# Performance work log

Measured on AMD Instinct MI355X. Metric: run time of the kernel, lower is better.

## Reference

```python
import jax, jax.numpy as jnp
import numpy as np

M, C = 100000, 24
LINE_W, LENGTH_W, REPROJ_W = 0.0, 0.0, 1.0  # forward() default weights


def setup_inputs() -> dict:
    ks = jax.random.split(jax.random.key(0), 8)
    # 3 pole markers per frame, centered ~5m in front of cameras (positive depth)
    pole3d = 0.5 * jax.random.normal(ks[0], (M, 3, 3), jnp.float32) + jnp.array([0.0, 0.0, 5.0], jnp.float32)
    # intrinsics: fx=fy~1000, principal point ~(960,540)
    fx = 1000.0 + 10.0 * jax.random.normal(ks[1], (C,), jnp.float32)
    fy = 1000.0 + 10.0 * jax.random.normal(ks[2], (C,), jnp.float32)
    u0 = 960.0 + 5.0 * jax.random.normal(ks[3], (C,), jnp.float32)
    v0 = 540.0 + 5.0 * jax.random.normal(ks[4], (C,), jnp.float32)
    K = jnp.zeros((C, 3, 3), jnp.float32)
    K = K.at[:, 0, 0].set(fx).at[:, 1, 1].set(fy).at[:, 0, 2].set(u0).at[:, 1, 2].set(v0).at[:, 2, 2].set(1.0)
    dist = 0.01 * jax.random.normal(ks[5], (C, 5), jnp.float32)  # k1,k2,p1,p2,k3
    R = jnp.eye(3, dtype=jnp.float32)[None] + 0.01 * jax.random.normal(ks[6], (C, 3, 3), jnp.float32)
    t = 0.1 * jax.random.normal(ks[7], (C, 3), jnp.float32)
    # detected pixels in a 1920x1080 frame
    pole2d = jax.random.uniform(jax.random.fold_in(ks[0], 1), (M, C, 3, 2), jnp.float32) * jnp.array([1920.0, 1080.0], jnp.float32)
    # visibility mask; guarantee >=1 visible camera per frame (matches non-empty loss_reproj)
    mask = jax.random.randint(jax.random.fold_in(ks[0], 2), (M, C), 0, 2, jnp.int32).at[:, 0].set(1)
    pole = jnp.array([0.5, 0.5], jnp.float32)  # [d1, d2] in meters
    return {"pole3d": pole3d, "pole2d": pole2d, "K": K, "dist": dist, "R": R, "t": t, "pole": pole, "mask": mask}


def _project(X, K, R, t, dist):
    # X: [M,P,3] world points; outputs pixels [M,C,P,2]
    xc = jnp.einsum('cij,mpj->mcpi', R, X) + t[None, :, None, :]   # camera frame
    xn = xc[..., :2] / xc[..., 2:3]                                # perspective divide
    x0, x1 = xn[..., 0], xn[..., 1]
    r2 = x0 * x0 + x1 * x1
    k1, k2, p1, p2, k3 = (dist[:, i][None, :, None] for i in range(5))
    radial = 1.0 + k1 * r2 + k2 * r2 * r2 + k3 * r2 * r2 * r2
    xu = x0 * radial + 2.0 * p1 * x0 * x1 + p2 * (r2 + 2.0 * x0 * x0)
    yu = x1 * radial + p1 * (r2 + 2.0 * x1 * x1) + 2.0 * p2 * x0 * x1
    fx = K[:, 0, 0][None, :, None]; fy = K[:, 1, 1][None, :, None]
    u0 = K[:, 0, 2][None, :, None]; v0 = K[:, 1, 2][None, :, None]
    return jnp.stack([fx * xu + u0, fy * yu + v0], axis=-1)


def reference(pole3d, pole2d, K, dist, R, t, pole, mask):
    d1, d2 = pole[0], pole[1]
    dsum = d1 + d2
    # wand geometry loss per frame
    expect_mid = (d2 * pole3d[:, 0] + d1 * pole3d[:, 2]) / dsum            # [M,3]
    loss_line = jnp.linalg.norm(pole3d[:, 1] - expect_mid, axis=-1)        # [M]
    loss_length = jnp.abs(jnp.linalg.norm(pole3d[:, 0] - pole3d[:, 2], axis=-1) - dsum)
    loss_wand = LINE_W * loss_line + LENGTH_W * loss_length                # [M]
    # reprojection loss
    proj = _project(pole3d, K, R, t, dist)                                 # [M,C,3,2]
    per_cam = REPROJ_W * jnp.linalg.norm(pole2d - proj, axis=-1).mean(axis=-1)  # [M,C]
    m = mask.astype(per_cam.dtype)
    loss_reproj = (per_cam * m).sum(axis=-1) / m.sum(axis=-1)              # masked mean over cams
    return jnp.mean(loss_wand + loss_reproj)
```

## Files before the change

kernel.cpp:

```cpp
#include <hip/hip_runtime.h>

#define MM 100000
#define CC 24
#define BLK 256
#define WPB (BLK / 64)
#define GRID 1280
#define NW (GRID * WPB)
#define NP (MM / 2)

struct Pack {
    float2 a0, a1, a2;
    float  w;
    float  q[9];
};

__device__ __forceinline__ Pack load_pack(
    const float* __restrict__ pole3d, const float* __restrict__ pole2d,
    const int* __restrict__ mask, int m, int c, float active)
{
    Pack pk;
    const float2* pd = (const float2*)(pole2d + ((size_t)m * CC + c) * 6);
    pk.a0 = pd[0]; pk.a1 = pd[1]; pk.a2 = pd[2];
    pk.w  = active * (float)mask[(size_t)m * CC + c];
    const float* q = pole3d + (size_t)m * 9;
    #pragma unroll
    for (int i = 0; i < 9; ++i) pk.q[i] = q[i];
    return pk;
}

__device__ __forceinline__ void pin(const Pack& p) {
    asm volatile("" ::
        "v"(p.a0.x), "v"(p.a0.y), "v"(p.a1.x), "v"(p.a1.y),
        "v"(p.a2.x), "v"(p.a2.y), "v"(p.w),
        "v"(p.q[0]), "v"(p.q[1]), "v"(p.q[2]), "v"(p.q[3]), "v"(p.q[4]),
        "v"(p.q[5]), "v"(p.q[6]), "v"(p.q[7]), "v"(p.q[8]));
}

__global__ __launch_bounds__(BLK) void ba_main_kernel(
    const float* __restrict__ pole3d,
    const float* __restrict__ pole2d,
    const float* __restrict__ Kmat,
    const float* __restrict__ dist,
    const float* __restrict__ Rmat,
    const float* __restrict__ tvec,
    const int*   __restrict__ mask,
    float* __restrict__ ws)
{
    const int tid  = threadIdx.x;
    const int lane = tid & 63;
    const int half = lane >> 5;
    const int cl   = lane & 31;
    const int c    = (cl < CC) ? cl : (CC - 1);
    const float active = (cl < CC) ? 1.f : 0.f;

    const float fx = Kmat[c * 9 + 0], fy = Kmat[c * 9 + 4];
    const float u0 = Kmat[c * 9 + 2], v0 = Kmat[c * 9 + 5];
    const float k1 = dist[c * 5 + 0], k2 = dist[c * 5 + 1];
    const float p1 = dist[c * 5 + 2], p2 = dist[c * 5 + 3], k3 = dist[c * 5 + 4];
    const float r00 = Rmat[c * 9 + 0], r01 = Rmat[c * 9 + 1], r02 = Rmat[c * 9 + 2];
    const float r10 = Rmat[c * 9 + 3], r11 = Rmat[c * 9 + 4], r12 = Rmat[c * 9 + 5];
    const float r20 = Rmat[c * 9 + 6], r21 = Rmat[c * 9 + 7], r22 = Rmat[c * 9 + 8];
    const float t0 = tvec[c * 3 + 0], t1 = tvec[c * 3 + 1], t2 = tvec[c * 3 + 2];

    const int wid = blockIdx.x * WPB + (tid >> 6);

    float acc = 0.f;

    Pack cur = load_pack(pole3d, pole2d, mask, 2 * wid + half, c, active);
    pin(cur);

    for (int p = wid; p < NP; p += NW) {
        const int pn = p + NW;
        const int pc = (pn < NP) ? pn : wid;
        Pack nxt = load_pack(pole3d, pole2d, mask, 2 * pc + half, c, active);
        pin(nxt);

        float s = 0.f;
        const float2 obs[3] = {cur.a0, cur.a1, cur.a2};
        #pragma unroll
        for (int i = 0; i < 3; ++i) {
            const float X = cur.q[3 * i + 0], Y = cur.q[3 * i + 1], Z = cur.q[3 * i + 2];
            const float xc = r00 * X + r01 * Y + r02 * Z + t0;
            const float yc = r10 * X + r11 * Y + r12 * Z + t1;
            const float zc = r20 * X + r21 * Y + r22 * Z + t2;
            const float inv = __builtin_amdgcn_rcpf(zc);
            const float x0 = xc * inv, x1 = yc * inv;
            const float r2 = x0 * x0 + x1 * x1;
            const float radial = 1.f + r2 * (k1 + r2 * (k2 + r2 * k3));
            const float xu = x0 * radial + 2.f * p1 * x0 * x1 + p2 * (r2 + 2.f * x0 * x0);
            const float yu = x1 * radial + p1 * (r2 + 2.f * x1 * x1) + 2.f * p2 * x0 * x1;
            const float u = fx * xu + u0;
            const float v = fy * yu + v0;
            const float dx = obs[i].x - u;
            const float dy = obs[i].y - v;
            s += __builtin_amdgcn_sqrtf(dx * dx + dy * dy);
        }

        const unsigned long long ball = __ballot(cur.w != 0.f);
        const unsigned wcnt = half ? __popcll(ball >> 32)
                                   : __popcll(ball & 0xFFFFFFFFull);
        acc += s * cur.w * __builtin_amdgcn_rcpf((float)(3u * wcnt));

        cur = nxt;
    }

    float tot = acc;
    #pragma unroll
    for (int d = 1; d < 64; d <<= 1) tot += __shfl_xor(tot, d);

    __shared__ float sh[WPB];
    if (lane == 0) sh[tid >> 6] = tot;
    __syncthreads();
    if (tid == 0) {
        float bl = 0.f;
        #pragma unroll
        for (int j = 0; j < WPB; ++j) bl += sh[j];
        ws[blockIdx.x] = bl;
    }
}

__global__ __launch_bounds__(256) void ba_reduce_kernel(
    const float* __restrict__ ws, float* __restrict__ out)
{
    __shared__ float sh[256];
    float s = 0.f;
    for (int i = threadIdx.x; i < GRID; i += 256) s += ws[i];
    sh[threadIdx.x] = s;
    __syncthreads();
    #pragma unroll
    for (int st = 128; st > 0; st >>= 1) {
        if (threadIdx.x < st) sh[threadIdx.x] += sh[threadIdx.x + st];
        __syncthreads();
    }
    if (threadIdx.x == 0) out[0] = sh[0] * (1.0f / MM);
}

extern "C" void kernel_launch(void* const* d_in, const int* in_sizes, int n_in,
                              void* d_out, int out_size, void* d_ws, size_t ws_size,
                              hipStream_t stream) {
    const float* pole3d = (const float*)d_in[0];
    const float* pole2d = (const float*)d_in[1];
    const float* Kmat   = (const float*)d_in[2];
    const float* dist   = (const float*)d_in[3];
    const float* Rmat   = (const float*)d_in[4];
    const float* tvec   = (const float*)d_in[5];
    const int*   mask   = (const int*)d_in[7];
    float* out = (float*)d_out;
    float* ws  = (float*)d_ws;

    ba_main_kernel<<<GRID, BLK, 0, stream>>>(
        pole3d, pole2d, Kmat, dist, Rmat, tvec, mask, ws);
    ba_reduce_kernel<<<1, 256, 0, stream>>>(ws, out);
}
```

Before: 27.72 us.

## Pack all 24 camera lanes densely and precompute per-frame inverse visible counts

Adds a pre-pass kernel that sums each frame's mask and stores 1/(3*count) in workspace. The main kernel now maps threads densely over (frame, camera) pairs, so no lanes are wasted. Previously each wave covered two frames with 32 lanes each, leaving 8 of every 32 idle, and used a ballot to count visible cameras. The old kernel is kept as a fallback for when the workspace is too small. The cost is an extra kernel launch and an extra pass over the mask, plus one more gather per thread.

```diff
diff --git a/kernel.cpp b/kernel.cpp
--- a/kernel.cpp
+++ b/kernel.cpp
@@ -3,40 +3,60 @@
 #define MM 100000
 #define CC 24
 #define BLK 256
-#define WPB (BLK / 64)
-#define GRID 1280
-#define NW (GRID * WPB)
-#define NP (MM / 2)
-
-struct Pack {
+#define GRID 1536
+#define NT (GRID * BLK)
+#define NT24 (NT / CC)
+#define INV_OFF 0
+#define PART_OFF 100096
+#define WS_NEED ((PART_OFF + GRID) * 4)
+
+
+__global__ __launch_bounds__(BLK) void ba_wcnt_kernel(
+    const int* __restrict__ mask, float* __restrict__ ws)
+{
+    const int f = blockIdx.x * BLK + threadIdx.x;
+    if (f >= MM) return;
+    const int4* mp = (const int4*)(mask + (size_t)f * CC);
+    int s = 0;
+    #pragma unroll
+    for (int i = 0; i < 6; ++i) {
+        const int4 v = mp[i];
+        s += v.x + v.y + v.z + v.w;
+    }
+    ws[INV_OFF + f] = __builtin_amdgcn_rcpf((float)(3 * s));
+}
+
+struct PackD {
     float2 a0, a1, a2;
     float  w;
+    float  iw;
     float  q[9];
 };
 
-__device__ __forceinline__ Pack load_pack(
+__device__ __forceinline__ PackD load_packd(
     const float* __restrict__ pole3d, const float* __restrict__ pole2d,
-    const int* __restrict__ mask, int m, int c, float active)
-{
-    Pack pk;
-    const float2* pd = (const float2*)(pole2d + ((size_t)m * CC + c) * 6);
+    const int* __restrict__ mask, const float* __restrict__ inv3w, int f, int c)
+{
+    PackD pk;
+    const float2* pd = (const float2*)(pole2d + ((size_t)f * CC + c) * 6);
     pk.a0 = pd[0]; pk.a1 = pd[1]; pk.a2 = pd[2];
-    pk.w  = active * (float)mask[(size_t)m * CC + c];
-    const float* q = pole3d + (size_t)m * 9;
+    pk.w  = (float)mask[(size_t)f * CC + c];
+    pk.iw = inv3w[f];
+    const float* q = pole3d + (size_t)f * 9;
     #pragma unroll
     for (int i = 0; i < 9; ++i) pk.q[i] = q[i];
     return pk;
 }
 
-__device__ __forceinline__ void pin(const Pack& p) {
+__device__ __forceinline__ void pind(const PackD& p) {
     asm volatile("" ::
         "v"(p.a0.x), "v"(p.a0.y), "v"(p.a1.x), "v"(p.a1.y),
-        "v"(p.a2.x), "v"(p.a2.y), "v"(p.w),
+        "v"(p.a2.x), "v"(p.a2.y), "v"(p.w), "v"(p.iw),
         "v"(p.q[0]), "v"(p.q[1]), "v"(p.q[2]), "v"(p.q[3]), "v"(p.q[4]),
         "v"(p.q[5]), "v"(p.q[6]), "v"(p.q[7]), "v"(p.q[8]));
 }
 
-__global__ __launch_bounds__(BLK) void ba_main_kernel(
+__global__ __launch_bounds__(BLK) void ba_dense_kernel(
     const float* __restrict__ pole3d,
     const float* __restrict__ pole2d,
     const float* __restrict__ Kmat,
@@ -44,14 +64,13 @@
     const float* __restrict__ Rmat,
     const float* __restrict__ tvec,
     const int*   __restrict__ mask,
-    float* __restrict__ ws)
-{
-    const int tid  = threadIdx.x;
-    const int lane = tid & 63;
-    const int half = lane >> 5;
-    const int cl   = lane & 31;
-    const int c    = (cl < CC) ? cl : (CC - 1);
-    const float active = (cl < CC) ? 1.f : 0.f;
+    const float* __restrict__ inv3w,
+    float* __restrict__ partials)
+{
+    const int tid = threadIdx.x;
+    const int g   = blockIdx.x * BLK + tid;
+    const int c   = g % CC;
+    const int f0  = g / CC;
 
     const float fx = Kmat[c * 9 + 0], fy = Kmat[c * 9 + 4];
     const float u0 = Kmat[c * 9 + 2], v0 = Kmat[c * 9 + 5];
@@ -62,18 +81,16 @@
     const float r20 = Rmat[c * 9 + 6], r21 = Rmat[c * 9 + 7], r22 = Rmat[c * 9 + 8];
     const float t0 = tvec[c * 3 + 0], t1 = tvec[c * 3 + 1], t2 = tvec[c * 3 + 2];
 
-    const int wid = blockIdx.x * WPB + (tid >> 6);
-
     float acc = 0.f;
 
-    Pack cur = load_pack(pole3d, pole2d, mask, 2 * wid + half, c, active);
-    pin(cur);
-
-    for (int p = wid; p < NP; p += NW) {
-        const int pn = p + NW;
-        const int pc = (pn < NP) ? pn : wid;
-        Pack nxt = load_pack(pole3d, pole2d, mask, 2 * pc + half, c, active);
-        pin(nxt);
+    PackD cur = load_packd(pole3d, pole2d, mask, inv3w, f0, c);
+    pind(cur);
+
+    for (int f = f0; f < MM; f += NT24) {
+        const int fn = f + NT24;
+        const int fp = (fn < MM) ? fn : f0;
+        PackD nxt = load_packd(pole3d, pole2d, mask, inv3w, fp, c);
+        pind(nxt);
 
         float s = 0.f;
         const float2 obs[3] = {cur.a0, cur.a1, cur.a2};
@@ -89,18 +106,13 @@
             const float radial = 1.f + r2 * (k1 + r2 * (k2 + r2 * k3));
             const float xu = x0 * radial + 2.f * p1 * x0 * x1 + p2 * (r2 + 2.f * x0 * x0);
             const float yu = x1 * radial + p1 * (r2 + 2.f * x1 * x1) + 2.f * p2 * x0 * x1;
-            const float u = fx * xu + u0;
-            const float v = fy * yu + v0;
-            const float dx = obs[i].x - u;
-            const float dy = obs[i].y - v;
+            const float uu = fx * xu + u0;
+            const float vv = fy * yu + v0;
+            const float dx = obs[i].x - uu;
+            const float dy = obs[i].y - vv;
             s += __builtin_amdgcn_sqrtf(dx * dx + dy * dy);
         }
-
-        const unsigned long long ball = __ballot(cur.w != 0.f);
-        const unsigned wcnt = half ? __popcll(ball >> 32)
-                                   : __popcll(ball & 0xFFFFFFFFull);
-        acc += s * cur.w * __builtin_amdgcn_rcpf((float)(3u * wcnt));
-
+        acc += s * cur.w * cur.iw;
         cur = nxt;
     }
 
@@ -108,23 +120,23 @@
     #pragma unroll
     for (int d = 1; d < 64; d <<= 1) tot += __shfl_xor(tot, d);
 
-    __shared__ float sh[WPB];
-    if (lane == 0) sh[tid >> 6] = tot;
+    __shared__ float sh[BLK / 64];
+    if ((tid & 63) == 0) sh[tid >> 6] = tot;
     __syncthreads();
     if (tid == 0) {
         float bl = 0.f;
         #pragma unroll
-        for (int j = 0; j < WPB; ++j) bl += sh[j];
-        ws[blockIdx.x] = bl;
+        for (int j = 0; j < BLK / 64; ++j) bl += sh[j];
+        partials[blockIdx.x] = bl;
     }
 }
 
 __global__ __launch_bounds__(256) void ba_reduce_kernel(
-    const float* __restrict__ ws, float* __restrict__ out)
+    const float* __restrict__ partials, int n, float* __restrict__ out)
 {
     __shared__ float sh[256];
     float s = 0.f;
-    for (int i = threadIdx.x; i < GRID; i += 256) s += ws[i];
+    for (int i = threadIdx.x; i < n; i += 256) s += partials[i];
     sh[threadIdx.x] = s;
     __syncthreads();
     #pragma unroll
@@ -134,6 +146,107 @@
     }
     if (threadIdx.x == 0) out[0] = sh[0] * (1.0f / MM);
 }
+
+
+#define FB_GRID 1280
+#define FB_NW (FB_GRID * 4)
+#define NP (MM / 2)
+
+struct Pack {
+    float2 a0, a1, a2; float w; float q[9];
+};
+
+__device__ __forceinline__ Pack load_pack(
+    const float* __restrict__ pole3d, const float* __restrict__ pole2d,
+    const int* __restrict__ mask, int m, int c, float active)
+{
+    Pack pk;
+    const float2* pd = (const float2*)(pole2d + ((size_t)m * CC + c) * 6);
+    pk.a0 = pd[0]; pk.a1 = pd[1]; pk.a2 = pd[2];
+    pk.w  = active * (float)mask[(size_t)m * CC + c];
+    const float* q = pole3d + (size_t)m * 9;
+    #pragma unroll
+    for (int i = 0; i < 9; ++i) pk.q[i] = q[i];
+    return pk;
+}
+
+__device__ __forceinline__ void pin(const Pack& p) {
+    asm volatile("" ::
+        "v"(p.a0.x), "v"(p.a0.y), "v"(p.a1.x), "v"(p.a1.y),
+        "v"(p.a2.x), "v"(p.a2.y), "v"(p.w),
+        "v"(p.q[0]), "v"(p.q[1]), "v"(p.q[2]), "v"(p.q[3]), "v"(p.q[4]),
+        "v"(p.q[5]), "v"(p.q[6]), "v"(p.q[7]), "v"(p.q[8]));
+}
+
+__global__ __launch_bounds__(BLK) void ba_fb_kernel(
+    const float* __restrict__ pole3d, const float* __restrict__ pole2d,
+    const float* __restrict__ Kmat, const float* __restrict__ dist,
+    const float* __restrict__ Rmat, const float* __restrict__ tvec,
+    const int* __restrict__ mask, float* __restrict__ ws)
+{
+    const int tid  = threadIdx.x;
+    const int lane = tid & 63;
+    const int half = lane >> 5;
+    const int cl   = lane & 31;
+    const int c    = (cl < CC) ? cl : (CC - 1);
+    const float active = (cl < CC) ? 1.f : 0.f;
+
+    const float fx = Kmat[c * 9 + 0], fy = Kmat[c * 9 + 4];
+    const float u0 = Kmat[c * 9 + 2], v0 = Kmat[c * 9 + 5];
+    const float k1 = dist[c * 5 + 0], k2 = dist[c * 5 + 1];
+    const float p1 = dist[c * 5 + 2], p2 = dist[c * 5 + 3], k3 = dist[c * 5 + 4];
+    const float r00 = Rmat[c * 9 + 0], r01 = Rmat[c * 9 + 1], r02 = Rmat[c * 9 + 2];
+    const float r10 = Rmat[c * 9 + 3], r11 = Rmat[c * 9 + 4], r12 = Rmat[c * 9 + 5];
+    const float r20 = Rmat[c * 9 + 6], r21 = Rmat[c * 9 + 7], r22 = Rmat[c * 9 + 8];
+    const float t0 = tvec[c * 3 + 0], t1 = tvec[c * 3 + 1], t2 = tvec[c * 3 + 2];
+
+    const int wid = blockIdx.x * 4 + (tid >> 6);
+    float acc = 0.f;
+    Pack cur = load_pack(pole3d, pole2d, mask, 2 * wid + half, c, active);
+    pin(cur);
+
+    for (int p = wid; p < NP; p += FB_NW) {
+        const int pn = p + FB_NW;
+        const int pc = (pn < NP) ? pn : wid;
+        Pack nxt = load_pack(pole3d, pole2d, mask, 2 * pc + half, c, active);
+        pin(nxt);
+
+        float s = 0.f;
+        const float2 obs[3] = {cur.a0, cur.a1, cur.a2};
+        #pragma unroll
+        for (int i = 0; i < 3; ++i) {
+            const float X = cur.q[3 * i + 0], Y = cur.q[3 * i + 1], Z = cur.q[3 * i + 2];
+            const float xc = r00 * X + r01 * Y + r02 * Z + t0;
+            const float yc = r10 * X + r11 * Y + r12 * Z + t1;
+            const float zc = r20 * X + r21 * Y + r22 * Z + t2;
+            const float inv = __builtin_amdgcn_rcpf(zc);
+            const float x0 = xc * inv, x1 = yc * inv;
+            const float r2 = x0 * x0 + x1 * x1;
+            const float radial = 1.f + r2 * (k1 + r2 * (k2 + r2 * k3));
+            const float xu = x0 * radial + 2.f * p1 * x0 * x1 + p2 * (r2 + 2.f * x0 * x0);
+            const float yu = x1 * radial + p1 * (r2 + 2.f * x1 * x1) + 2.f * p2 * x0 * x1;
+            const float uu = fx * xu + u0;
+            const float vv = fy * yu + v0;
+            const float dx = obs[i].x - uu;
+            const float dy = obs[i].y - vv;
+            s += __builtin_amdgcn_sqrtf(dx * dx + dy * dy);
+        }
+        const unsigned long long ball = __ballot(cur.w != 0.f);
+        const unsigned wcnt = half ? __popcll(ball >> 32) : __popcll(ball & 0xFFFFFFFFull);
+        acc += s * cur.w * __builtin_amdgcn_rcpf((float)(3u * wcnt));
+        cur = nxt;
+    }
+
+    float tot = acc;
+    #pragma unroll
+    for (int d = 1; d < 64; d <<= 1) tot += __shfl_xor(tot, d);
+
+    __shared__ float sh[4];
+    if (lane == 0) sh[tid >> 6] = tot;
+    __syncthreads();
+    if (tid == 0) ws[blockIdx.x] = sh[0] + sh[1] + sh[2] + sh[3];
+}
+
 
 extern "C" void kernel_launch(void* const* d_in, const int* in_sizes, int n_in,
                               void* d_out, int out_size, void* d_ws, size_t ws_size,
@@ -148,7 +261,15 @@
     float* out = (float*)d_out;
     float* ws  = (float*)d_ws;
 
-    ba_main_kernel<<<GRID, BLK, 0, stream>>>(
-        pole3d, pole2d, Kmat, dist, Rmat, tvec, mask, ws);
-    ba_reduce_kernel<<<1, 256, 0, stream>>>(ws, out);
-}
+    if (ws_size >= (size_t)WS_NEED) {
+        ba_wcnt_kernel<<<(MM + BLK - 1) / BLK, BLK, 0, stream>>>(mask, ws + INV_OFF);
+        ba_dense_kernel<<<GRID, BLK, 0, stream>>>(
+            pole3d, pole2d, Kmat, dist, Rmat, tvec, mask,
+            ws + INV_OFF, ws + PART_OFF);
+        ba_reduce_kernel<<<1, 256, 0, stream>>>(ws + PART_OFF, GRID, out);
+    } else {
+        ba_fb_kernel<<<FB_GRID, BLK, 0, stream>>>(
+            pole3d, pole2d, Kmat, dist, Rmat, tvec, mask, ws);
+        ba_reduce_kernel<<<1, 256, 0, stream>>>(ws, FB_GRID, out);
+    }
+}
```

Result: slower. 29.42 us (+6.1%).
